# Kernel tuning notes

Measured on AMD Instinct MI355X. Metric: run time of the kernel, lower is better.

## Reference

```python
import jax, jax.numpy as jnp
import numpy as np

EMB = 768
HEADS = 12
B, N = 32, 1024


def setup_inputs() -> dict:
    key = jax.random.key(0)
    ks = jax.random.split(key, 7)
    s = 1.0 / np.sqrt(EMB)
    return {
        "x": jax.random.normal(ks[0], (B, N, EMB), dtype=jnp.float32),
        "Wq": jax.random.normal(ks[1], (EMB, EMB), dtype=jnp.float32) * s,
        "bq": jnp.zeros((EMB,), dtype=jnp.float32),
        "Wk": jax.random.normal(ks[2], (EMB, EMB), dtype=jnp.float32) * s,
        "bk": jnp.zeros((EMB,), dtype=jnp.float32),
        "Wv": jax.random.normal(ks[3], (EMB, EMB), dtype=jnp.float32) * s,
        "bv": jnp.zeros((EMB,), dtype=jnp.float32),
    }


def reference(x, Wq, bq, Wk, bk, Wv, bv):
    b, n, _ = x.shape
    h = HEADS
    e = EMB // h  # head dim
    # project and split heads: b n (h e) -> b h n e
    def split(t):
        return t.reshape(b, n, h, e).transpose(0, 2, 1, 3)
    q = split(x @ Wq + bq)
    k = split(x @ Wk + bk)
    v = split(x @ Wv + bv)
    # NOTE: scale is 1/sqrt(num_head), as in the original module
    wei = jnp.einsum('bhie,bhje->bhij', q, k) / jnp.sqrt(jnp.float32(h))
    # NOTE: softmax over dim=2 = query axis i (non-standard)
    wei = jax.nn.softmax(wei, axis=2)
    # dropout is identity in eval mode
    out = jnp.einsum('bhij,bhje->bhie', wei, v)
    return out.transpose(0, 2, 1, 3).reshape(b, n, h * e)
```

## Files before the change

### kernel.cpp

```cpp
#include <hip/hip_runtime.h>

#define EMB 768
#define NH 12
#define HD 64
#define BB 32
#define NN 1024
#define QSCALE 0.41647025f

typedef _Float16 h8 __attribute__((ext_vector_type(8)));
typedef _Float16 h4 __attribute__((ext_vector_type(4)));
typedef _Float16 h2 __attribute__((ext_vector_type(2)));
typedef float f4 __attribute__((ext_vector_type(4)));

static __device__ __forceinline__ f4 mfma16(h8 a, h8 b, f4 c) {
  return __builtin_amdgcn_mfma_f32_16x16x32_f16(a, b, c, 0, 0, 0);
}

static __device__ __forceinline__ h2 cvt_pk(float a, float b) {
  return __builtin_bit_cast(h2, __builtin_amdgcn_cvt_pkrtz(a, b));
}

static __device__ __forceinline__ float exp2a(float x) {
#if __has_builtin(__builtin_amdgcn_exp2f)
  return __builtin_amdgcn_exp2f(x);
#else
  float r;
  asm("v_exp_f32 %0, %1\n\ts_nop 1" : "=v"(r) : "v"(x));
  return r;
#endif
}

static __device__ __forceinline__ void gload16(const _Float16* g, _Float16* lds) {
  __builtin_amdgcn_global_load_lds(
      (const __attribute__((address_space(1))) void*)g,
      (__attribute__((address_space(3))) void*)lds, 16, 0, 0);
}

__global__ __launch_bounds__(256) void k_cvt(const float* __restrict__ X,
                                             _Float16* __restrict__ Xh, int n4) {
  int i = blockIdx.x * 256 + threadIdx.x;
  if (i >= n4) return;
  float4 v = ((const float4*)X)[i];
  h4 o = {(_Float16)v.x, (_Float16)v.y, (_Float16)v.z, (_Float16)v.w};
  ((h4*)Xh)[i] = o;
}

__global__ __launch_bounds__(256) void k_wt(const float* __restrict__ W0,
                                            const float* __restrict__ W1,
                                            const float* __restrict__ W2,
                                            _Float16* __restrict__ Wt) {
  const float* W = blockIdx.z == 0 ? W0 : (blockIdx.z == 1 ? W1 : W2);
  _Float16* dst = Wt + (size_t)blockIdx.z * EMB * EMB;
  __shared__ float tile[64][65];
  const int t = threadIdx.x;
  const int r0 = blockIdx.y * 64, c0 = blockIdx.x * 64;
  const int r = t >> 4, c4 = (t & 15) * 4;
#pragma unroll
  for (int i = 0; i < 4; ++i) {
    const float4 v = *(const float4*)&W[(size_t)(r0 + r + 16 * i) * EMB + c0 + c4];
    tile[r + 16 * i][c4 + 0] = v.x; tile[r + 16 * i][c4 + 1] = v.y;
    tile[r + 16 * i][c4 + 2] = v.z; tile[r + 16 * i][c4 + 3] = v.w;
  }
  __syncthreads();
  const int cc = t >> 2, rr = (t & 3) * 16;
#pragma unroll
  for (int half = 0; half < 2; ++half) {
    h8 o;
#pragma unroll
    for (int j = 0; j < 8; ++j) o[j] = (_Float16)tile[rr + half * 8 + j][cc];
    *(h8*)&dst[(size_t)(c0 + cc) * EMB + r0 + rr + half * 8] = o;
  }
}

__global__ __launch_bounds__(256) void k_projf(const _Float16* __restrict__ Xh,
                                               const _Float16* __restrict__ Wt,
                                               const float* __restrict__ bq,
                                               const float* __restrict__ bk,
                                               const float* __restrict__ bv,
                                               _Float16* __restrict__ Qw,
                                               _Float16* __restrict__ Kw,
                                               _Float16* __restrict__ Vtmp) {
  __shared__ _Float16 As[2][128 * 64];
  __shared__ _Float16 Bs[2][128 * 64];
  const int t = threadIdx.x;
  const int w = t >> 6, l = t & 63;
  const int wm = w >> 1, wn = w & 1;
  const int p = l & 15, g = l >> 4;
  const int by = blockIdx.x;
  const int m0 = blockIdx.y * 128;
  const int n0 = by * 128;

  f4 acc[4][4];
#pragma unroll
  for (int mf = 0; mf < 4; ++mf)
#pragma unroll
    for (int nf = 0; nf < 4; ++nf) acc[mf][nf] = f4{0.f, 0.f, 0.f, 0.f};

  const int lrow = l >> 3, lch = (l & 7) ^ (l >> 3);

#define STAGE(buf, k0)                                                            \
  {                                                                               \
    _Float16* ab = &As[buf][0];                                                   \
    _Float16* bb = &Bs[buf][0];                                                   \
    _Pragma("unroll") for (int i = 0; i < 4; ++i) {                               \
      const int seg = (w << 2) | i;                                               \
      const int grow = (seg << 3) | lrow;                                         \
      gload16(Xh + (size_t)(m0 + grow) * EMB + (k0) + lch * 8, ab + seg * 512);   \
      gload16(Wt + (size_t)(n0 + grow) * EMB + (k0) + lch * 8, bb + seg * 512);   \
    }                                                                             \
  }

  STAGE(0, 0)
  __syncthreads();

  int cur = 0;
  for (int kt = 0; kt < 12; ++kt) {
    if (kt + 1 < 12) STAGE(cur ^ 1, (kt + 1) * 64)
    const char* asb = (const char*)&As[cur][0];
    const char* bsb = (const char*)&Bs[cur][0];
#pragma unroll
    for (int ks = 0; ks < 2; ++ks) {
      h8 af[4], bf[4];
#pragma unroll
      for (int mf = 0; mf < 4; ++mf)
        af[mf] = *(const h8*)(asb + ((wm * 64 + mf * 16 + p) << 7) +
                              ((((ks << 2) | g) ^ (p & 7)) << 4));
#pragma unroll
      for (int nf = 0; nf < 4; ++nf)
        bf[nf] = *(const h8*)(bsb + ((wn * 64 + nf * 16 + p) << 7) +
                              ((((ks << 2) | g) ^ (p & 7)) << 4));
#pragma unroll
      for (int mf = 0; mf < 4; ++mf)
#pragma unroll
        for (int nf = 0; nf < 4; ++nf) acc[mf][nf] = mfma16(af[mf], bf[nf], acc[mf][nf]);
    }
    __syncthreads();
    cur ^= 1;
  }
#undef STAGE

  const int z = by / 6;
  const int nl0 = (by % 6) * 128;
  const float* bias = z == 0 ? bq : (z == 1 ? bk : bv);
  _Float16* Outz = z == 0 ? Qw : (z == 1 ? Kw : Vtmp);
  const float scale = z == 0 ? QSCALE : 1.0f;
#pragma unroll
  for (int nf = 0; nf < 4; ++nf) {
    const int C = nl0 + wn * 64 + nf * 16 + p;
    const float bvv = bias[C];
    const int h = C >> 6, e = C & 63;
#pragma unroll
    for (int mf = 0; mf < 4; ++mf) {
#pragma unroll
      for (int r = 0; r < 4; ++r) {
        const int R = m0 + wm * 64 + mf * 16 + g * 4 + r;
        const int b = R >> 10, tok = R & 1023;
        Outz[((size_t)(b * NH + h) * NN + tok) * HD + e] = (_Float16)((acc[mf][nf][r] + bvv) * scale);
      }
    }
  }
}

__global__ __launch_bounds__(256) void k_stats(const _Float16* __restrict__ Q,
                                               const _Float16* __restrict__ K,
                                               const _Float16* __restrict__ Vtmp,
                                               float* __restrict__ MT,
                                               _Float16* __restrict__ Vt) {
  const int bh = blockIdx.x * 48 + (blockIdx.y >> 3);
  const int jt = blockIdx.y & 7;
  const int j0 = jt * 128;
  __shared__ __align__(16) char SMEM[50704];
  _Float16* Ks   = (_Float16*)SMEM;
  _Float16* Qs0  = (_Float16*)(SMEM + 16384);
  _Float16* Qs1  = (_Float16*)(SMEM + 32768);
  float* Lj      = (float*)(SMEM + 49152);
  float* reds    = (float*)(SMEM + 49664);
  float* MsShp   = (float*)(SMEM + 50688);
  _Float16 (*Vtile)[72] = (_Float16(*)[72])SMEM;
  _Float16* qsBuf[2] = {Qs0, Qs1};
  const _Float16* Qb = Q + (size_t)bh * NN * HD;
  const _Float16* Kb = K + (size_t)bh * NN * HD;
  const int t = threadIdx.x, w = t >> 6, l = t & 63;
  const int wi = w >> 1, wj = w & 1;
  const int p = l & 15, g = l >> 4;
  const int lrow = l >> 3, lch = (l & 7) ^ (l >> 3);

#define STAGEQ(dst, i0v)                                                          \
  {                                                                               \
    _Pragma("unroll") for (int i = 0; i < 4; ++i) {                               \
      const int seg = (w << 2) | i;                                               \
      const int grow = (seg << 3) | lrow;                                         \
      gload16(Qb + (size_t)((i0v) + grow) * HD + lch * 8, (dst) + seg * 512);     \
    }                                                                             \
  }

#pragma unroll
  for (int i = 0; i < 4; ++i) {
    const int seg = (w << 2) | i;
    const int grow = (seg << 3) | lrow;
    gload16(Kb + (size_t)(j0 + grow) * HD + lch * 8, Ks + seg * 512);
  }
  STAGEQ(Qs0, 0)
  if (t < 128) Lj[t] = 0.f;
  __syncthreads();

  const char* ksb = (const char*)Ks;
  int cur = 0;
  for (int i0 = 0; i0 < NN; i0 += 128) {
    if (i0 + 128 < NN) STAGEQ(qsBuf[cur ^ 1], i0 + 128)
    const char* qsb = (const char*)qsBuf[cur];
    f4 s[4][4];
#pragma unroll
    for (int mf = 0; mf < 4; ++mf)
#pragma unroll
      for (int nf = 0; nf < 4; ++nf) s[mf][nf] = f4{0.f, 0.f, 0.f, 0.f};
#pragma unroll
    for (int ks = 0; ks < 2; ++ks) {
      h8 af[4], bf[4];
#pragma unroll
      for (int mf = 0; mf < 4; ++mf)
        af[mf] = *(const h8*)(qsb + ((wi * 64 + mf * 16 + p) << 7) + ((((ks << 2) | g) ^ (p & 7)) << 4));
#pragma unroll
      for (int nf = 0; nf < 4; ++nf)
        bf[nf] = *(const h8*)(ksb + ((wj * 64 + nf * 16 + p) << 7) + ((((ks << 2) | g) ^ (p & 7)) << 4));
#pragma unroll
      for (int mf = 0; mf < 4; ++mf)
#pragma unroll
        for (int nf = 0; nf < 4; ++nf) s[mf][nf] = mfma16(af[mf], bf[nf], s[mf][nf]);
    }
#pragma unroll
    for (int nf = 0; nf < 4; ++nf) {
      float cs = 0.f;
#pragma unroll
      for (int mf = 0; mf < 4; ++mf)
#pragma unroll
        for (int r = 0; r < 4; ++r) cs += exp2a(s[mf][nf][r]);
      cs += __shfl_xor(cs, 16);
      cs += __shfl_xor(cs, 32);
      if (l < 16) reds[wi * 128 + wj * 64 + nf * 16 + l] = cs;
    }
    __syncthreads();
    if (t < 128) Lj[t] += reds[t] + reds[128 + t];
    __syncthreads();
    cur ^= 1;
  }
#undef STAGEQ
  if (w == 0) {
    float mv = fmaxf(Lj[l], Lj[l + 64]);
#pragma unroll
    for (int d = 32; d; d >>= 1) mv = fmaxf(mv, __shfl_xor(mv, d));
    if (l == 0) { MsShp[0] = __log2f(mv); MT[bh * 8 + jt] = MsShp[0]; }
  }
  __syncthreads();
  const float rmsc = exp2a(MsShp[0]);

  const _Float16* Vb = Vtmp + (size_t)bh * NN * HD;
  _Float16* Vo = Vt + (size_t)bh * HD * NN;
  const int jr = t >> 3, c8 = (t & 7) * 8;
#pragma unroll
  for (int half = 0; half < 2; ++half) {
#pragma unroll
    for (int i = 0; i < 2; ++i) {
      const int jl = half * 64 + jr + 32 * i;
      const float inv = rmsc / Lj[jl];
      h8 v = *(const h8*)&Vb[(size_t)(j0 + jl) * HD + c8];
      h8 o;
#pragma unroll
      for (int j = 0; j < 8; ++j) o[j] = (_Float16)((float)v[j] * inv);
      *(h8*)&Vtile[jr + 32 * i][c8] = o;
    }
    __syncthreads();
#pragma unroll
    for (int i = 0; i < 2; ++i) {
      h8 o;
#pragma unroll
      for (int j = 0; j < 8; ++j) o[j] = Vtile[c8 + j][jr + 32 * i];
      *(h8*)&Vo[(size_t)(jr + 32 * i) * NN + j0 + half * 64 + c8] = o;
    }
    __syncthreads();
  }
}

__global__ __launch_bounds__(256) void k_out(const _Float16* __restrict__ Q,
                                             const _Float16* __restrict__ K,
                                             const _Float16* __restrict__ Vt,
                                             const float* __restrict__ MT,
                                             float* __restrict__ Out) {
  const int bh = blockIdx.x * 48 + (blockIdx.y >> 2);
  const int i0 = (blockIdx.y & 3) * 256;
  const int b = bh / NH, h = bh % NH;
  __shared__ _Float16 Ks[2][32][64];
  __shared__ _Float16 Vts[2][64][32];
  __shared__ _Float16 Ps[4][2][32][32];
  const _Float16* Qb = Q + (size_t)bh * NN * HD;
  const _Float16* Kb = K + (size_t)bh * NN * HD;
  const _Float16* Vb = Vt + (size_t)bh * HD * NN;
  const int t = threadIdx.x, w = t >> 6, l = t & 63;
  const int p = l & 15, g = l >> 4;
  char* psb[2] = {(char*)&Ps[w][0][0][0], (char*)&Ps[w][1][0][0]};

  h8 bq[2][2][2];
#pragma unroll
  for (int it = 0; it < 2; ++it)
#pragma unroll
    for (int f = 0; f < 2; ++f)
#pragma unroll
      for (int ks = 0; ks < 2; ++ks)
        bq[it][f][ks] = *(const h8*)&Qb[(size_t)(i0 + it * 128 + w * 32 + f * 16 + p) * HD + ks * 32 + g * 8];

  f4 oacc[2][4][2];
#pragma unroll
  for (int it = 0; it < 2; ++it)
#pragma unroll
    for (int ef = 0; ef < 4; ++ef)
#pragma unroll
      for (int f = 0; f < 2; ++f) oacc[it][ef][f] = f4{0.f, 0.f, 0.f, 0.f};

  const int kr = t >> 3, kc = t & 7;
  const int vr = t >> 2, vc = t & 3;

  h8 kreg = *(const h8*)&Kb[(size_t)kr * HD + kc * 8];
  h8 vreg = *(const h8*)&Vb[(size_t)vr * NN + vc * 8];
  *(h8*)((char*)&Ks[0][0][0] + (kr << 7) + ((kc ^ (kr & 7)) << 4)) = kreg;
  *(h8*)((char*)&Vts[0][0][0] + (vr << 6) + ((vc ^ ((vr >> 1) & 3)) << 4)) = vreg;

  for (int jt4 = 0; jt4 < 8; ++jt4) {
    const float Mstar = MT[bh * 8 + jt4];
#pragma unroll
    for (int u = 0; u < 4; ++u) {
      const int jt = jt4 * 4 + u;
      const int cur = u & 1;
      char* ksb = (char*)&Ks[cur][0][0];
      char* vsb = (char*)&Vts[cur][0][0];
      __syncthreads();
      if (jt + 1 < 32) {
        const int j0n = (jt + 1) * 32;
        kreg = *(const h8*)&Kb[(size_t)(j0n + kr) * HD + kc * 8];
        vreg = *(const h8*)&Vb[(size_t)vr * NN + j0n + vc * 8];
      }

      h8 ak[2][2], av[4];
#pragma unroll
      for (int ks = 0; ks < 2; ++ks)
#pragma unroll
        for (int jf = 0; jf < 2; ++jf)
          ak[ks][jf] = *(const h8*)(ksb + ((jf * 16 + p) << 7) + ((((ks << 2) | g) ^ (p & 7)) << 4));
#pragma unroll
      for (int ef = 0; ef < 4; ++ef)
        av[ef] = *(const h8*)(vsb + ((ef * 16 + p) << 6) + ((g ^ ((p >> 1) & 3)) << 4));

#pragma unroll
      for (int it = 0; it < 2; ++it) {
        f4 s[2][2];
#pragma unroll
        for (int f = 0; f < 2; ++f)
#pragma unroll
          for (int jf = 0; jf < 2; ++jf) s[f][jf] = f4{-Mstar, -Mstar, -Mstar, -Mstar};
#pragma unroll
        for (int ks = 0; ks < 2; ++ks)
#pragma unroll
          for (int f = 0; f < 2; ++f)
#pragma unroll
            for (int jf = 0; jf < 2; ++jf) s[f][jf] = mfma16(ak[ks][jf], bq[it][f][ks], s[f][jf]);
#pragma unroll
        for (int f = 0; f < 2; ++f)
#pragma unroll
          for (int jf = 0; jf < 2; ++jf) {
            const f4 sv = s[f][jf];
            h2 lo = cvt_pk(exp2a(sv[0]), exp2a(sv[1]));
            h2 hi = cvt_pk(exp2a(sv[2]), exp2a(sv[3]));
            h4 pw; pw[0] = lo[0]; pw[1] = lo[1]; pw[2] = hi[0]; pw[3] = hi[1];
            *(h4*)(psb[it] + ((f * 16 + p) << 6) +
                   (((2 * jf + (g >> 1)) ^ ((p >> 1) & 3)) << 4) + ((g & 1) << 3)) = pw;
          }
      }
      asm volatile("s_waitcnt lgkmcnt(0)" ::: "memory");
      __builtin_amdgcn_sched_barrier(0);

#pragma unroll
      for (int it = 0; it < 2; ++it) {
        h8 bp[2];
#pragma unroll
        for (int f = 0; f < 2; ++f)
          bp[f] = *(const h8*)(psb[it] + ((f * 16 + p) << 6) + ((g ^ ((p >> 1) & 3)) << 4));
#pragma unroll
        for (int ef = 0; ef < 4; ++ef)
#pragma unroll
          for (int f = 0; f < 2; ++f) oacc[it][ef][f] = mfma16(av[ef], bp[f], oacc[it][ef][f]);
      }

      if (jt + 1 < 32) {
        *(h8*)((char*)&Ks[cur ^ 1][0][0] + (kr << 7) + ((kc ^ (kr & 7)) << 4)) = kreg;
        *(h8*)((char*)&Vts[cur ^ 1][0][0] + (vr << 6) + ((vc ^ ((vr >> 1) & 3)) << 4)) = vreg;
      }
    }
  }

#pragma unroll
  for (int it = 0; it < 2; ++it) {
#pragma unroll
    for (int f = 0; f < 2; ++f) {
      const int i = i0 + it * 128 + w * 32 + f * 16 + p;
#pragma unroll
      for (int ef = 0; ef < 4; ++ef) {
        float4 o4 = {oacc[it][ef][f][0], oacc[it][ef][f][1], oacc[it][ef][f][2], oacc[it][ef][f][3]};
        *(float4*)&Out[((size_t)b * NN + i) * EMB + h * HD + ef * 16 + 4 * g] = o4;
      }
    }
  }
}

extern "C" void kernel_launch(void* const* d_in, const int* in_sizes, int n_in,
                              void* d_out, int out_size, void* d_ws, size_t ws_size,
                              hipStream_t stream) {
  const float* X  = (const float*)d_in[0];
  const float* Wq = (const float*)d_in[1];
  const float* bq = (const float*)d_in[2];
  const float* Wk = (const float*)d_in[3];
  const float* bk = (const float*)d_in[4];
  const float* Wv = (const float*)d_in[5];
  const float* bv = (const float*)d_in[6];

  char* ws = (char*)d_ws;
  _Float16* Qw = (_Float16*)(ws);
  _Float16* Kw = (_Float16*)(ws + 50331648);
  _Float16* Vt = (_Float16*)(ws + 100663296);
  _Float16* Wt = (_Float16*)(ws + 150994944);
  float* MT    = (float*)(ws + 154533888);

  _Float16* Xh   = (_Float16*)d_out;
  _Float16* Vtmp = (_Float16*)((char*)d_out + 50331648);
  float* Out = (float*)d_out;

  k_cvt<<<dim3(6291456 / 256), 256, 0, stream>>>(X, Xh, 6291456);
  k_wt<<<dim3(12, 12, 3), 256, 0, stream>>>(Wq, Wk, Wv, Wt);
  k_projf<<<dim3(18, 256), 256, 0, stream>>>(Xh, Wt, bq, bk, bv, Qw, Kw, Vtmp);
  k_stats<<<dim3(8, 384), 256, 0, stream>>>(Qw, Kw, Vtmp, MT, Vt);
  k_out<<<dim3(8, 192), 256, 0, stream>>>(Qw, Kw, Vt, MT, Out);
}
```

Before: 387.7 us.

## Restructure projection GEMM with 256x128 tiles, triple-buffered LDS and phased MFMA

```diff
diff --git a/kernel.cpp b/kernel.cpp
--- a/kernel.cpp
+++ b/kernel.cpp
@@ -72,7 +72,7 @@
   }
 }
 
-__global__ __launch_bounds__(256) void k_projf(const _Float16* __restrict__ Xh,
+__global__ __launch_bounds__(512) void k_projf(const _Float16* __restrict__ Xh,
                                                const _Float16* __restrict__ Wt,
                                                const float* __restrict__ bq,
                                                const float* __restrict__ bk,
@@ -80,14 +80,19 @@
                                                _Float16* __restrict__ Qw,
                                                _Float16* __restrict__ Kw,
                                                _Float16* __restrict__ Vtmp) {
-  __shared__ _Float16 As[2][128 * 64];
-  __shared__ _Float16 Bs[2][128 * 64];
+  extern __shared__ __align__(16) _Float16 smem[];
+  _Float16* Ab = smem;
+  _Float16* Bb = smem + 49152;
+  const char* abase = (const char*)Ab;
+  const char* bbase = (const char*)Bb;
   const int t = threadIdx.x;
   const int w = t >> 6, l = t & 63;
   const int wm = w >> 1, wn = w & 1;
   const int p = l & 15, g = l >> 4;
-  const int by = blockIdx.x;
-  const int m0 = blockIdx.y * 128;
+  int bid = (int)blockIdx.x;
+  bid = (bid & 7) * 288 + (bid >> 3);
+  const int my = bid / 18, by = bid % 18;
+  const int m0 = my * 256;
   const int n0 = by * 128;
 
   f4 acc[4][4];
@@ -98,46 +103,77 @@
 
   const int lrow = l >> 3, lch = (l & 7) ^ (l >> 3);
 
-#define STAGE(buf, k0)                                                            \
-  {                                                                               \
-    _Float16* ab = &As[buf][0];                                                   \
-    _Float16* bb = &Bs[buf][0];                                                   \
-    _Pragma("unroll") for (int i = 0; i < 4; ++i) {                               \
-      const int seg = (w << 2) | i;                                               \
-      const int grow = (seg << 3) | lrow;                                         \
-      gload16(Xh + (size_t)(m0 + grow) * EMB + (k0) + lch * 8, ab + seg * 512);   \
-      gload16(Wt + (size_t)(n0 + grow) * EMB + (k0) + lch * 8, bb + seg * 512);   \
-    }                                                                             \
-  }
-
-  STAGE(0, 0)
-  __syncthreads();
-
-  int cur = 0;
+#define SA2(bufS, k2, half)                                                        \
+  {                                                                                \
+    _Pragma("unroll") for (int i = 0; i < 2; ++i) {                                \
+      const int seg = (w << 2) | ((half) << 1) | i;                                \
+      const int grow = (seg << 3) | lrow;                                          \
+      gload16(Xh + (size_t)(m0 + grow) * EMB + (k2) + lch * 8,                     \
+              Ab + (bufS) * 16384 + seg * 512);                                    \
+    }                                                                              \
+  }
+#define SB1(bufS, k2, half)                                                        \
+  {                                                                                \
+    const int seg = (w << 1) | (half);                                             \
+    const int grow = (seg << 3) | lrow;                                            \
+    gload16(Wt + (size_t)(n0 + grow) * EMB + (k2) + lch * 8,                       \
+            Bb + (bufS) * 8192 + seg * 512);                                       \
+  }
+
+#define PHASE(bufR, mh, nh, STAGE_STMT, TAIL_STMT)                                 \
+  {                                                                                \
+    h8 af[2][2], bf[2][2];                                                         \
+    _Pragma("unroll") for (int mi = 0; mi < 2; ++mi)                               \
+      _Pragma("unroll") for (int ks = 0; ks < 2; ++ks)                             \
+        af[mi][ks] = *(const h8*)(abase + (bufR) * 32768 +                         \
+            ((wm * 64 + ((mh) * 2 + mi) * 16 + p) << 7) +                          \
+            ((((ks << 2) | g) ^ (p & 7)) << 4));                                   \
+    _Pragma("unroll") for (int ni = 0; ni < 2; ++ni)                               \
+      _Pragma("unroll") for (int ks = 0; ks < 2; ++ks)                             \
+        bf[ni][ks] = *(const h8*)(bbase + (bufR) * 16384 +                         \
+            ((wn * 64 + ((nh) * 2 + ni) * 16 + p) << 7) +                          \
+            ((((ks << 2) | g) ^ (p & 7)) << 4));                                   \
+    STAGE_STMT;                                                                    \
+    __builtin_amdgcn_s_barrier();                                                  \
+    asm volatile("s_waitcnt lgkmcnt(0)" ::: "memory");                             \
+    __builtin_amdgcn_sched_barrier(0);                                             \
+    __builtin_amdgcn_s_setprio(1);                                                 \
+    _Pragma("unroll") for (int ks = 0; ks < 2; ++ks)                               \
+      _Pragma("unroll") for (int mi = 0; mi < 2; ++mi)                             \
+        _Pragma("unroll") for (int ni = 0; ni < 2; ++ni)                           \
+          acc[(mh) * 2 + mi][(nh) * 2 + ni] =                                      \
+              mfma16(af[mi][ks], bf[ni][ks], acc[(mh) * 2 + mi][(nh) * 2 + ni]);   \
+    __builtin_amdgcn_s_setprio(0);                                                 \
+    TAIL_STMT;                                                                     \
+    __builtin_amdgcn_s_barrier();                                                  \
+  }
+
+  SA2(0, 0, 0) SA2(0, 0, 1) SB1(0, 0, 0) SB1(0, 0, 1)
+  SA2(1, 64, 0) SA2(1, 64, 1) SB1(1, 64, 0) SB1(1, 64, 1)
+  asm volatile("s_waitcnt vmcnt(6)" ::: "memory");
+  __builtin_amdgcn_s_barrier();
+
+#pragma unroll
   for (int kt = 0; kt < 12; ++kt) {
-    if (kt + 1 < 12) STAGE(cur ^ 1, (kt + 1) * 64)
-    const char* asb = (const char*)&As[cur][0];
-    const char* bsb = (const char*)&Bs[cur][0];
-#pragma unroll
-    for (int ks = 0; ks < 2; ++ks) {
-      h8 af[4], bf[4];
-#pragma unroll
-      for (int mf = 0; mf < 4; ++mf)
-        af[mf] = *(const h8*)(asb + ((wm * 64 + mf * 16 + p) << 7) +
-                              ((((ks << 2) | g) ^ (p & 7)) << 4));
-#pragma unroll
-      for (int nf = 0; nf < 4; ++nf)
-        bf[nf] = *(const h8*)(bsb + ((wn * 64 + nf * 16 + p) << 7) +
-                              ((((ks << 2) | g) ^ (p & 7)) << 4));
-#pragma unroll
-      for (int mf = 0; mf < 4; ++mf)
-#pragma unroll
-        for (int nf = 0; nf < 4; ++nf) acc[mf][nf] = mfma16(af[mf], bf[nf], acc[mf][nf]);
-    }
-    __syncthreads();
-    cur ^= 1;
-  }
-#undef STAGE
+    const int bufR = kt % 3;
+    const int bufS = (kt + 2) % 3;
+    const int k2 = (kt + 2) * 64;
+    const bool st = (kt + 2) < 12;
+    PHASE(bufR, 0, 0, if (st) SA2(bufS, k2, 0), )
+    PHASE(bufR, 0, 1, if (st) SA2(bufS, k2, 1), )
+    PHASE(bufR, 1, 0, if (st) SB1(bufS, k2, 0), )
+    if (kt < 10) {
+      PHASE(bufR, 1, 1, if (st) SB1(bufS, k2, 1),
+            asm volatile("s_waitcnt vmcnt(6)" ::: "memory"))
+    } else if (kt == 10) {
+      PHASE(bufR, 1, 1, , asm volatile("s_waitcnt vmcnt(0)" ::: "memory"))
+    } else {
+      PHASE(bufR, 1, 1, , )
+    }
+  }
+#undef PHASE
+#undef SA2
+#undef SB1
 
   const int z = by / 6;
   const int nl0 = (by % 6) * 128;
@@ -432,9 +468,16 @@
   _Float16* Vtmp = (_Float16*)((char*)d_out + 50331648);
   float* Out = (float*)d_out;
 
+  static int lds_set = 0;
+  if (!lds_set) {
+    hipFuncSetAttribute((const void*)k_projf,
+                        hipFuncAttributeMaxDynamicSharedMemorySize, 147456);
+    lds_set = 1;
+  }
+
   k_cvt<<<dim3(6291456 / 256), 256, 0, stream>>>(X, Xh, 6291456);
   k_wt<<<dim3(12, 12, 3), 256, 0, stream>>>(Wq, Wk, Wv, Wt);
-  k_projf<<<dim3(18, 256), 256, 0, stream>>>(Xh, Wt, bq, bk, bv, Qw, Kw, Vtmp);
+  k_projf<<<dim3(2304), 512, 147456, stream>>>(Xh, Wt, bq, bk, bv, Qw, Kw, Vtmp);
   k_stats<<<dim3(8, 384), 256, 0, stream>>>(Qw, Kw, Vtmp, MT, Vt);
   k_out<<<dim3(8, 192), 256, 0, stream>>>(Qw, Kw, Vt, MT, Out);
 }
```

Result: no change. 390.1 us (+0.6%).
